# Performance work log

Measured on AMD Instinct MI355X. Metric: run time of the kernel, lower is better.

Reference implementation:

```python
import jax, jax.numpy as jnp
from jax import lax
import numpy as np

SLOPE = 0.1  # LeakyReLU negative slope used throughout DA_conv


def setup_inputs() -> dict:
    key = jax.random.key(0)
    ks = jax.random.split(key, 8)
    B, C, H, W = 16, 64, 160, 160
    Cout, red = 64, 8
    feat = jax.random.normal(ks[0], (B, C, H, W), dtype=jnp.float32)
    deg = jax.random.normal(ks[1], (B, C, 1, 1), dtype=jnp.float32)
    W1 = jax.random.normal(ks[2], (64, C), dtype=jnp.float32) * 0.05
    W2 = jax.random.normal(ks[3], (Cout * 9, 64), dtype=jnp.float32) * 0.05
    Wc = jax.random.normal(ks[4], (Cout, Cout), dtype=jnp.float32) * 0.05
    bc = jnp.zeros((Cout,), dtype=jnp.float32)
    Wd1 = jax.random.normal(ks[5], (red, C), dtype=jnp.float32) * 0.05
    Wd2 = jax.random.normal(ks[6], (Cout, red), dtype=jnp.float32) * 0.05
    return {"feat": feat, "deg": deg, "W1": W1, "W2": W2, "Wc": Wc,
            "bc": bc, "Wd1": Wd1, "Wd2": Wd2}


def reference(feat, deg, W1, W2, Wc, bc, Wd1, Wd2):
    B, C, H, W = feat.shape
    Cout = Wc.shape[0]
    KS = 3
    d = deg[:, :, 0, 0]  # [B, C]

    # --- dynamic per-sample, per-channel 3x3 kernel generation ---
    h = jax.nn.leaky_relu(d @ W1.T, SLOPE)            # [B, 64]
    k = (h @ W2.T).reshape(B * Cout, 1, KS, KS)        # [B*Cout, 1, 3, 3]

    # grouped depthwise conv: input [1, B*C, H, W], groups = B*C
    x = feat.reshape(1, B * C, H, W)
    out = lax.conv_general_dilated(
        x, k, window_strides=(1, 1), padding=[(1, 1), (1, 1)],
        dimension_numbers=("NCHW", "OIHW", "NCHW"),
        feature_group_count=B * C)
    out = jax.nn.leaky_relu(out, SLOPE).reshape(B, Cout, H, W)

    # 1x1 conv with bias (common.default_conv)
    out = jnp.einsum("oi,bihw->bohw", Wc, out) + bc[None, :, None, None]

    # --- channel attention branch (1x1 convs == matmuls on [B,C]) ---
    a = jax.nn.leaky_relu(jnp.einsum("ri,bi->br", Wd1, d), SLOPE)   # [B, red]
    att = jax.nn.sigmoid(jnp.einsum("or,br->bo", Wd2, a))           # [B, Cout]

    return out + feat * att[:, :, None, None]
```

## Files before the change

kernel.cpp:

```cpp
#include <hip/hip_runtime.h>
#include <hip/hip_bf16.h>
#include <math.h>

#define SLOPE 0.1f
#define B_ 16
#define C_ 64
#define H_ 160
#define W_ 160
#define HW_ (H_*W_)

typedef short bf16x8 __attribute__((ext_vector_type(8)));
typedef float f32x4  __attribute__((ext_vector_type(4)));
typedef unsigned int uint2v __attribute__((ext_vector_type(2)));

__device__ __forceinline__ float lrelu(float x) { return fmaxf(x, SLOPE * x); }
__device__ __forceinline__ unsigned f2bf(float x) {
  union { float f; unsigned u; } c; c.f = x;
  return (c.u + 0x7fffu + ((c.u >> 16) & 1u)) >> 16;
}
__device__ __forceinline__ float bf2f(unsigned short u) {
  union { unsigned u; float f; } c; c.u = ((unsigned)u) << 16; return c.f;
}

__device__ __forceinline__ void gl2lds16(const void* g, void* l) {
  __builtin_amdgcn_global_load_lds(
      (const __attribute__((address_space(1))) void*)g,
      (__attribute__((address_space(3))) void*)l, 16, 0, 0);
}

__global__ __launch_bounds__(64) void prep_kernel(
    const float* __restrict__ deg,
    const float* __restrict__ W1,
    const float* __restrict__ W2,
    const float* __restrict__ Wd1,
    const float* __restrict__ Wd2,
    float* __restrict__ ws) {
  const int b = blockIdx.x;
  const int j = threadIdx.x;
  __shared__ float sd[64], sh[64], sa[8];
  sd[j] = deg[b * 64 + j];
  __syncthreads();

  float acc = 0.f;
  for (int i = 0; i < 64; ++i) acc = fmaf(sd[i], W1[j * 64 + i], acc);
  sh[j] = lrelu(acc);

  if (j < 8) {
    float s = 0.f;
    for (int i = 0; i < 64; ++i) s = fmaf(sd[i], Wd1[j * 64 + i], s);
    sa[j] = lrelu(s);
  }
  __syncthreads();

  float kv[9];
#pragma unroll
  for (int t = 0; t < 9; ++t) kv[t] = 0.f;
  for (int l = 0; l < 64; ++l) {
    float hl = sh[l];
#pragma unroll
    for (int t = 0; t < 9; ++t) kv[t] = fmaf(hl, W2[(j * 9 + t) * 64 + l], kv[t]);
  }
  unsigned short* kw = (unsigned short*)(ws + 1024) + (b * 64 + j) * 16;
#pragma unroll
  for (int t = 0; t < 9; ++t) kw[t] = (unsigned short)f2bf(kv[t]);
#pragma unroll
  for (int t = 9; t < 16; ++t) kw[t] = 0;

  float s2 = 0.f;
#pragma unroll
  for (int r = 0; r < 8; ++r) s2 = fmaf(Wd2[j * 8 + r], sa[r], s2);
  ws[b * 64 + j] = 1.f / (1.f + __expf(-s2));
}

__global__ __launch_bounds__(256, 4) void main_kernel(
    const float* __restrict__ feat,
    const float* __restrict__ Wc,
    const float* __restrict__ bc,
    const float* __restrict__ ws,
    float* __restrict__ out) {
  __shared__ __align__(16) float S[2][16][240];
  __shared__ __align__(16) unsigned short Tt[2048];
  __shared__ __align__(16) unsigned short Ff[2048];
  __shared__ __align__(16) unsigned short Kl[1024];

  const int rb  = blockIdx.x;
  const int bid = (rb & 7) * 400 + (rb >> 3);
  const int b   = bid / 200;
  const int rem = bid - b * 200;
  const int ty  = rem / 10, tx = rem - ty * 10;
  const int x0 = tx * 16, y0 = ty * 8;
  const int tid = threadIdx.x;
  const int lane = tid & 63, wid = tid >> 6;

  const float* __restrict__ attp  = ws + b * 64;
  const char*  __restrict__ kb8   = (const char*)(ws + 1024) + b * 2048;
  const float* __restrict__ plane = feat + (size_t)(b * 64) * HW_;

  const int ci = tid >> 4;
  const int q  = (tid >> 2) & 3;
  const int h  = tid & 3;
  const int nl = lane & 15, kg = lane >> 4;
  const int ochunk = wid * 16;

  const int srow = lane / 6;
  const int schk = lane - srow * 6;
  const int grow = min(max(y0 + srow - 1, 0), H_ - 1);
  const int gcol = min(max(x0 - 4 + schk * 4, 0), W_ - 4);
  const float* sp0 = plane + grow * W_ + gcol;

  union AF { bf16x8 v; unsigned short u[8]; };
  AF a[4];
#pragma unroll
  for (int g = 0; g < 4; ++g) {
    const float4 w = *(const float4*)(Wc + (ochunk + nl) * 64 + g * 16 + 4 * kg);
    a[g].u[0] = (unsigned short)f2bf(w.x); a[g].u[1] = (unsigned short)f2bf(w.y);
    a[g].u[2] = (unsigned short)f2bf(w.z); a[g].u[3] = (unsigned short)f2bf(w.w);
    a[g].u[4] = 0; a[g].u[5] = 0; a[g].u[6] = 0; a[g].u[7] = 0;
  }
  AF a2;
  {
    const unsigned short ab = (unsigned short)f2bf(attp[ochunk + nl]);
#pragma unroll
    for (int j = 0; j < 4; ++j) a2.u[j] = (nl == 4 * kg + j) ? ab : (unsigned short)0;
    a2.u[4] = 0; a2.u[5] = 0; a2.u[6] = 0; a2.u[7] = 0;
  }
  const float4 bcv = *(const float4*)(bc + ochunk + 4 * kg);

  asm volatile("s_waitcnt vmcnt(0)" ::: "memory");

  if (wid == 0) {
    gl2lds16(kb8 + lane * 16, &Kl[0]);
    gl2lds16(kb8 + 1024 + lane * 16, &Kl[512]);
  }
#define STAGE(g, bf) \
  if (lane < 60) { \
    const float* s_ = sp0 + (size_t)((g) * 16 + wid * 4) * HW_; \
    gl2lds16(s_,              &S[bf][wid * 4 + 0][0]); \
    gl2lds16(s_ + 1 * HW_,    &S[bf][wid * 4 + 1][0]); \
    gl2lds16(s_ + 2 * HW_,    &S[bf][wid * 4 + 2][0]); \
    gl2lds16(s_ + 3 * HW_,    &S[bf][wid * 4 + 3][0]); \
  }
  STAGE(0, 0);

  f32x4 acc[8];
#pragma unroll
  for (int nt = 0; nt < 8; ++nt) acc[nt] = (f32x4){0.f, 0.f, 0.f, 0.f};

  const float mlz = (x0 == 0 && q == 0) ? 0.f : 1.f;
  const float mrz = (x0 == W_ - 16 && q == 3) ? 0.f : 1.f;

  const unsigned t_base = (unsigned)(uintptr_t)&Tt[0] + (unsigned)(lane * 8);
  const unsigned f_base = (unsigned)(uintptr_t)&Ff[0] + (unsigned)(lane * 8);
  union BU { bf16x8 v; uint2v qv[2]; };

#pragma unroll
  for (int g = 0; g < 4; ++g) {
    const int bf = g & 1;
    if (g < 3) { STAGE(g + 1, bf ^ 1); }
    if (g < 3) asm volatile("s_waitcnt vmcnt(4)" ::: "memory");
    else       asm volatile("s_waitcnt vmcnt(0)" ::: "memory");
    __builtin_amdgcn_s_barrier();
    __builtin_amdgcn_sched_barrier(0);

    const unsigned short* kr = &Kl[(g * 16 + ci) * 16];
    union KU { uint4 v; unsigned short u[8]; } k07;
    k07.v = *(const uint4*)kr;
    const unsigned short k8u = kr[8];
    float kk[9];
#pragma unroll
    for (int t = 0; t < 8; ++t) kk[t] = bf2f(k07.u[t]);
    kk[8] = bf2f(k8u);

    float rv[4][9];
#pragma unroll
    for (int rr = 0; rr < 4; ++rr) {
      const float* sp = &S[bf][ci][(2 * h + rr) * 24 + 4 * q];
      const f32x4 v0 = *(const f32x4*)sp;
      const f32x4 v1 = *(const f32x4*)(sp + 4);
      rv[rr][0] = v0[0]; rv[rr][1] = v0[1]; rv[rr][2] = v0[2];
      rv[rr][3] = v0[3] * mlz;
      rv[rr][4] = v1[0]; rv[rr][5] = v1[1]; rv[rr][6] = v1[2]; rv[rr][7] = v1[3];
      rv[rr][8] = sp[8] * mrz;
    }

#pragma unroll
    for (int rr = 0; rr < 2; ++rr) {
      const int srw = 2 * h + rr;
      const float mt = (srw == 0 && y0 == 0) ? 0.f : 1.f;
      const float mb = (srw == 7 && y0 == H_ - 8) ? 0.f : 1.f;
      float sv[4], fv[4];
#pragma unroll
      for (int j = 0; j < 4; ++j) {
        float ts = fmaf(rv[rr][j + 5], kk[2], fmaf(rv[rr][j + 4], kk[1], rv[rr][j + 3] * kk[0]));
        float cs = fmaf(rv[rr + 1][j + 5], kk[5], fmaf(rv[rr + 1][j + 4], kk[4], rv[rr + 1][j + 3] * kk[3]));
        float bs = fmaf(rv[rr + 2][j + 5], kk[8], fmaf(rv[rr + 2][j + 4], kk[7], rv[rr + 2][j + 3] * kk[6]));
        sv[j] = fmaf(mt, ts, fmaf(mb, bs, cs));
        fv[j] = rv[rr + 1][j + 4];
      }
      uint2v tq, fq;
      tq.x = f2bf(lrelu(sv[0])) | (f2bf(lrelu(sv[1])) << 16);
      tq.y = f2bf(lrelu(sv[2])) | (f2bf(lrelu(sv[3])) << 16);
      fq.x = f2bf(fv[0]) | (f2bf(fv[1]) << 16);
      fq.y = f2bf(fv[2]) | (f2bf(fv[3]) << 16);
      const int tidx = srw * 256 + ci * 16 + 4 * q;
      *(uint2v*)&Tt[tidx] = tq;
      *(uint2v*)&Ff[tidx] = fq;
    }

    asm volatile("s_waitcnt lgkmcnt(0)" ::: "memory");
    __builtin_amdgcn_s_barrier();
    __builtin_amdgcn_sched_barrier(0);

    uint2v tr[8];
#pragma unroll
    for (int nt = 0; nt < 8; ++nt)
      asm volatile("ds_read_b64_tr_b16 %0, %1 offset:%2"
                   : "=v"(tr[nt]) : "v"(t_base), "i"(nt * 512));
    if (wid == g) {
      uint2v fr[8];
#pragma unroll
      for (int nt = 0; nt < 8; ++nt)
        asm volatile("ds_read_b64_tr_b16 %0, %1 offset:%2"
                     : "=v"(fr[nt]) : "v"(f_base), "i"(nt * 512));
      asm volatile("s_waitcnt lgkmcnt(8)" ::: "memory");
      __builtin_amdgcn_sched_barrier(0);
#pragma unroll
      for (int nt = 0; nt < 8; ++nt) {
        BU bu; bu.qv[0] = tr[nt]; bu.qv[1] = (uint2v){0u, 0u};
        acc[nt] = __builtin_amdgcn_mfma_f32_16x16x32_bf16(a[g].v, bu.v, acc[nt], 0, 0, 0);
      }
      asm volatile("s_waitcnt lgkmcnt(0)" ::: "memory");
      __builtin_amdgcn_sched_barrier(0);
#pragma unroll
      for (int nt = 0; nt < 8; ++nt) {
        BU bu; bu.qv[0] = fr[nt]; bu.qv[1] = (uint2v){0u, 0u};
        acc[nt] = __builtin_amdgcn_mfma_f32_16x16x32_bf16(a2.v, bu.v, acc[nt], 0, 0, 0);
      }
    } else {
      asm volatile("s_waitcnt lgkmcnt(0)" ::: "memory");
      __builtin_amdgcn_sched_barrier(0);
#pragma unroll
      for (int nt = 0; nt < 8; ++nt) {
        BU bu; bu.qv[0] = tr[nt]; bu.qv[1] = (uint2v){0u, 0u};
        acc[nt] = __builtin_amdgcn_mfma_f32_16x16x32_bf16(a[g].v, bu.v, acc[nt], 0, 0, 0);
      }
    }
    __builtin_amdgcn_s_barrier();
    __builtin_amdgcn_sched_barrier(0);
  }
#undef STAGE

  const int ob = ochunk + 4 * kg;
  float* __restrict__ outb = out + (size_t)(b * 64) * HW_;
#pragma unroll
  for (int nt = 0; nt < 8; ++nt) {
    const int off = (y0 + nt) * W_ + x0 + nl;
    outb[(size_t)(ob + 0) * HW_ + off] = acc[nt][0] + bcv.x;
    outb[(size_t)(ob + 1) * HW_ + off] = acc[nt][1] + bcv.y;
    outb[(size_t)(ob + 2) * HW_ + off] = acc[nt][2] + bcv.z;
    outb[(size_t)(ob + 3) * HW_ + off] = acc[nt][3] + bcv.w;
  }
}

extern "C" void kernel_launch(void* const* d_in, const int* in_sizes, int n_in,
                              void* d_out, int out_size, void* d_ws, size_t ws_size,
                              hipStream_t stream) {
  const float* feat = (const float*)d_in[0];
  const float* deg  = (const float*)d_in[1];
  const float* W1   = (const float*)d_in[2];
  const float* W2   = (const float*)d_in[3];
  const float* Wc   = (const float*)d_in[4];
  const float* bc   = (const float*)d_in[5];
  const float* Wd1  = (const float*)d_in[6];
  const float* Wd2  = (const float*)d_in[7];
  float* out = (float*)d_out;
  float* ws  = (float*)d_ws;

  prep_kernel<<<dim3(B_), dim3(64), 0, stream>>>(deg, W1, W2, Wd1, Wd2, ws);
  main_kernel<<<dim3(3200), dim3(256), 0, stream>>>(feat, Wc, bc, ws, out);
}
```

Baseline: 74.13 us.

## Apply attention residual in fp32 epilogue and double-buffer depthwise tile to drop barrier

Drops the Ff bf16 feature tile and the extra MFMA pass with the diagonal attention matrix. The owning wave now reads residual feature values straight from the fp32 staging buffer and adds feat*att in the epilogue with an FMA, which also keeps the residual in full precision. The Tt buffer is double-buffered by stage parity so the barrier at the top of each iteration can go, and the per-sample kernel weights are repacked into a compact 12-element per-wave layout. This costs 32 extra registers for the residual and more LDS for the doubled Tt, and depends on the barrier reordering staying race-free.

```diff
diff --git a/kernel.cpp b/kernel.cpp
--- a/kernel.cpp
+++ b/kernel.cpp
@@ -60,11 +60,11 @@
 #pragma unroll
     for (int t = 0; t < 9; ++t) kv[t] = fmaf(hl, W2[(j * 9 + t) * 64 + l], kv[t]);
   }
-  unsigned short* kw = (unsigned short*)(ws + 1024) + (b * 64 + j) * 16;
+  const int slot = ((j & 15) >> 2) * 16 + (j >> 4) * 4 + (j & 3);
+  unsigned short* kw = (unsigned short*)((char*)ws + 4096) + b * 768 + slot * 12;
 #pragma unroll
   for (int t = 0; t < 9; ++t) kw[t] = (unsigned short)f2bf(kv[t]);
-#pragma unroll
-  for (int t = 9; t < 16; ++t) kw[t] = 0;
+  kw[9] = 0; kw[10] = 0; kw[11] = 0;
 
   float s2 = 0.f;
 #pragma unroll
@@ -78,10 +78,9 @@
     const float* __restrict__ bc,
     const float* __restrict__ ws,
     float* __restrict__ out) {
-  __shared__ __align__(16) float S[2][16][240];
-  __shared__ __align__(16) unsigned short Tt[2048];
-  __shared__ __align__(16) unsigned short Ff[2048];
-  __shared__ __align__(16) unsigned short Kl[1024];
+  __shared__ __align__(16) float S[2][16][244];
+  __shared__ __align__(16) unsigned short Tt[4096];
+  __shared__ __align__(16) unsigned short Kl[768];
 
   const int rb  = blockIdx.x;
   const int bid = (rb & 7) * 400 + (rb >> 3);
@@ -93,7 +92,7 @@
   const int lane = tid & 63, wid = tid >> 6;
 
   const float* __restrict__ attp  = ws + b * 64;
-  const char*  __restrict__ kb8   = (const char*)(ws + 1024) + b * 2048;
+  const char*  __restrict__ kb8   = (const char*)ws + 4096 + b * 1536;
   const float* __restrict__ plane = feat + (size_t)(b * 64) * HW_;
 
   const int ci = tid >> 4;
@@ -112,69 +111,70 @@
   AF a[4];
 #pragma unroll
   for (int g = 0; g < 4; ++g) {
-    const float4 w = *(const float4*)(Wc + (ochunk + nl) * 64 + g * 16 + 4 * kg);
-    a[g].u[0] = (unsigned short)f2bf(w.x); a[g].u[1] = (unsigned short)f2bf(w.y);
-    a[g].u[2] = (unsigned short)f2bf(w.z); a[g].u[3] = (unsigned short)f2bf(w.w);
+    const f32x4 w = *(const f32x4*)(Wc + (ochunk + nl) * 64 + g * 16 + 4 * kg);
+    a[g].u[0] = (unsigned short)f2bf(w[0]); a[g].u[1] = (unsigned short)f2bf(w[1]);
+    a[g].u[2] = (unsigned short)f2bf(w[2]); a[g].u[3] = (unsigned short)f2bf(w[3]);
     a[g].u[4] = 0; a[g].u[5] = 0; a[g].u[6] = 0; a[g].u[7] = 0;
   }
-  AF a2;
-  {
-    const unsigned short ab = (unsigned short)f2bf(attp[ochunk + nl]);
-#pragma unroll
-    for (int j = 0; j < 4; ++j) a2.u[j] = (nl == 4 * kg + j) ? ab : (unsigned short)0;
-    a2.u[4] = 0; a2.u[5] = 0; a2.u[6] = 0; a2.u[7] = 0;
-  }
-  const float4 bcv = *(const float4*)(bc + ochunk + 4 * kg);
-
+  const f32x4 bcv = *(const f32x4*)(bc + ochunk + 4 * kg);
+  const f32x4 atv = *(const f32x4*)(attp + ochunk + 4 * kg);
+  asm volatile("" :: "v"(a[0].v), "v"(a[1].v), "v"(a[2].v), "v"(a[3].v),
+                     "v"(bcv), "v"(atv));
   asm volatile("s_waitcnt vmcnt(0)" ::: "memory");
 
-  if (wid == 0) {
-    gl2lds16(kb8 + lane * 16, &Kl[0]);
-    gl2lds16(kb8 + 1024 + lane * 16, &Kl[512]);
-  }
-#define STAGE(g, bf) \
+  if (lane < 24) gl2lds16(kb8 + wid * 384 + lane * 16, &Kl[wid * 192]);
+#define STAGE(g_, bf_) \
   if (lane < 60) { \
-    const float* s_ = sp0 + (size_t)((g) * 16 + wid * 4) * HW_; \
-    gl2lds16(s_,              &S[bf][wid * 4 + 0][0]); \
-    gl2lds16(s_ + 1 * HW_,    &S[bf][wid * 4 + 1][0]); \
-    gl2lds16(s_ + 2 * HW_,    &S[bf][wid * 4 + 2][0]); \
-    gl2lds16(s_ + 3 * HW_,    &S[bf][wid * 4 + 3][0]); \
+    const float* s_ = sp0 + (size_t)((g_) * 16 + wid * 4) * HW_; \
+    gl2lds16(s_,            &S[bf_][wid * 4 + 0][0]); \
+    gl2lds16(s_ + HW_,      &S[bf_][wid * 4 + 1][0]); \
+    gl2lds16(s_ + 2 * HW_,  &S[bf_][wid * 4 + 2][0]); \
+    gl2lds16(s_ + 3 * HW_,  &S[bf_][wid * 4 + 3][0]); \
   }
   STAGE(0, 0);
 
   f32x4 acc[8];
 #pragma unroll
   for (int nt = 0; nt < 8; ++nt) acc[nt] = (f32x4){0.f, 0.f, 0.f, 0.f};
+  float resid[8][4];
+#pragma unroll
+  for (int nt = 0; nt < 8; ++nt)
+#pragma unroll
+    for (int j = 0; j < 4; ++j) resid[nt][j] = 0.f;
 
   const float mlz = (x0 == 0 && q == 0) ? 0.f : 1.f;
   const float mrz = (x0 == W_ - 16 && q == 3) ? 0.f : 1.f;
 
-  const unsigned t_base = (unsigned)(uintptr_t)&Tt[0] + (unsigned)(lane * 8);
-  const unsigned f_base = (unsigned)(uintptr_t)&Ff[0] + (unsigned)(lane * 8);
+  const unsigned t_lds0 = (unsigned)(uintptr_t)&Tt[0] + (unsigned)(lane * 8);
+  const unsigned t_lds1 = t_lds0 + 4096u;
   union BU { bf16x8 v; uint2v qv[2]; };
 
 #pragma unroll
   for (int g = 0; g < 4; ++g) {
-    const int bf = g & 1;
-    if (g < 3) { STAGE(g + 1, bf ^ 1); }
-    if (g < 3) asm volatile("s_waitcnt vmcnt(4)" ::: "memory");
-    else       asm volatile("s_waitcnt vmcnt(0)" ::: "memory");
-    __builtin_amdgcn_s_barrier();
-    __builtin_amdgcn_sched_barrier(0);
-
-    const unsigned short* kr = &Kl[(g * 16 + ci) * 16];
-    union KU { uint4 v; unsigned short u[8]; } k07;
-    k07.v = *(const uint4*)kr;
+    const int sb = g & 1;
+    if (g < 3) {
+      STAGE(g + 1, (g + 1) & 1);
+      asm volatile("s_waitcnt vmcnt(4)" ::: "memory");
+    } else {
+      asm volatile("s_waitcnt vmcnt(0)" ::: "memory");
+    }
+    __builtin_amdgcn_sched_barrier(0);
+
+    const unsigned short* kr = &Kl[wid * 192 + g * 48 + (lane >> 4) * 12];
+    union KU { uint2v v; unsigned short u[4]; };
+    KU kA, kB;
+    kA.v = *(const uint2v*)(kr);
+    kB.v = *(const uint2v*)(kr + 4);
     const unsigned short k8u = kr[8];
     float kk[9];
 #pragma unroll
-    for (int t = 0; t < 8; ++t) kk[t] = bf2f(k07.u[t]);
+    for (int t = 0; t < 4; ++t) { kk[t] = bf2f(kA.u[t]); kk[4 + t] = bf2f(kB.u[t]); }
     kk[8] = bf2f(k8u);
 
     float rv[4][9];
 #pragma unroll
     for (int rr = 0; rr < 4; ++rr) {
-      const float* sp = &S[bf][ci][(2 * h + rr) * 24 + 4 * q];
+      const float* sp = &S[sb][ci][(2 * h + rr) * 24 + 4 * q];
       const f32x4 v0 = *(const f32x4*)sp;
       const f32x4 v1 = *(const f32x4*)(sp + 4);
       rv[rr][0] = v0[0]; rv[rr][1] = v0[1]; rv[rr][2] = v0[2];
@@ -188,26 +188,22 @@
       const int srw = 2 * h + rr;
       const float mt = (srw == 0 && y0 == 0) ? 0.f : 1.f;
       const float mb = (srw == 7 && y0 == H_ - 8) ? 0.f : 1.f;
-      float sv[4], fv[4];
+      float sv[4];
 #pragma unroll
       for (int j = 0; j < 4; ++j) {
         float ts = fmaf(rv[rr][j + 5], kk[2], fmaf(rv[rr][j + 4], kk[1], rv[rr][j + 3] * kk[0]));
         float cs = fmaf(rv[rr + 1][j + 5], kk[5], fmaf(rv[rr + 1][j + 4], kk[4], rv[rr + 1][j + 3] * kk[3]));
         float bs = fmaf(rv[rr + 2][j + 5], kk[8], fmaf(rv[rr + 2][j + 4], kk[7], rv[rr + 2][j + 3] * kk[6]));
         sv[j] = fmaf(mt, ts, fmaf(mb, bs, cs));
-        fv[j] = rv[rr + 1][j + 4];
       }
-      uint2v tq, fq;
+      uint2v tq;
       tq.x = f2bf(lrelu(sv[0])) | (f2bf(lrelu(sv[1])) << 16);
       tq.y = f2bf(lrelu(sv[2])) | (f2bf(lrelu(sv[3])) << 16);
-      fq.x = f2bf(fv[0]) | (f2bf(fv[1]) << 16);
-      fq.y = f2bf(fv[2]) | (f2bf(fv[3]) << 16);
-      const int tidx = srw * 256 + ci * 16 + 4 * q;
-      *(uint2v*)&Tt[tidx] = tq;
-      *(uint2v*)&Ff[tidx] = fq;
+      *(uint2v*)&Tt[sb * 2048 + srw * 256 + ci * 16 + 4 * q] = tq;
     }
 
     asm volatile("s_waitcnt lgkmcnt(0)" ::: "memory");
+    __builtin_amdgcn_sched_barrier(0);
     __builtin_amdgcn_s_barrier();
     __builtin_amdgcn_sched_barrier(0);
 
@@ -215,38 +211,28 @@
 #pragma unroll
     for (int nt = 0; nt < 8; ++nt)
       asm volatile("ds_read_b64_tr_b16 %0, %1 offset:%2"
-                   : "=v"(tr[nt]) : "v"(t_base), "i"(nt * 512));
+                   : "=v"(tr[nt]) : "v"(sb ? t_lds1 : t_lds0), "i"(nt * 512));
+
     if (wid == g) {
-      uint2v fr[8];
+      volatile const float* Sv = &S[sb][0][0];
 #pragma unroll
       for (int nt = 0; nt < 8; ++nt)
-        asm volatile("ds_read_b64_tr_b16 %0, %1 offset:%2"
-                     : "=v"(fr[nt]) : "v"(f_base), "i"(nt * 512));
-      asm volatile("s_waitcnt lgkmcnt(8)" ::: "memory");
-      __builtin_amdgcn_sched_barrier(0);
-#pragma unroll
-      for (int nt = 0; nt < 8; ++nt) {
-        BU bu; bu.qv[0] = tr[nt]; bu.qv[1] = (uint2v){0u, 0u};
-        acc[nt] = __builtin_amdgcn_mfma_f32_16x16x32_bf16(a[g].v, bu.v, acc[nt], 0, 0, 0);
-      }
+#pragma unroll
+        for (int j = 0; j < 4; ++j)
+          resid[nt][j] = Sv[(4 * kg + j) * 244 + (nt + 1) * 24 + 4 + nl];
       asm volatile("s_waitcnt lgkmcnt(0)" ::: "memory");
-      __builtin_amdgcn_sched_barrier(0);
-#pragma unroll
-      for (int nt = 0; nt < 8; ++nt) {
-        BU bu; bu.qv[0] = fr[nt]; bu.qv[1] = (uint2v){0u, 0u};
-        acc[nt] = __builtin_amdgcn_mfma_f32_16x16x32_bf16(a2.v, bu.v, acc[nt], 0, 0, 0);
-      }
-    } else {
-      asm volatile("s_waitcnt lgkmcnt(0)" ::: "memory");
-      __builtin_amdgcn_sched_barrier(0);
-#pragma unroll
-      for (int nt = 0; nt < 8; ++nt) {
-        BU bu; bu.qv[0] = tr[nt]; bu.qv[1] = (uint2v){0u, 0u};
-        acc[nt] = __builtin_amdgcn_mfma_f32_16x16x32_bf16(a[g].v, bu.v, acc[nt], 0, 0, 0);
-      }
-    }
+    }
+    __builtin_amdgcn_sched_barrier(0);
     __builtin_amdgcn_s_barrier();
     __builtin_amdgcn_sched_barrier(0);
+    asm volatile("s_waitcnt lgkmcnt(0)" ::: "memory");
+    __builtin_amdgcn_sched_barrier(0);
+
+#pragma unroll
+    for (int nt = 0; nt < 8; ++nt) {
+      BU bu; bu.qv[0] = tr[nt]; bu.qv[1] = (uint2v){0u, 0u};
+      acc[nt] = __builtin_amdgcn_mfma_f32_16x16x32_bf16(a[g].v, bu.v, acc[nt], 0, 0, 0);
+    }
   }
 #undef STAGE
 
@@ -255,10 +241,10 @@
 #pragma unroll
   for (int nt = 0; nt < 8; ++nt) {
     const int off = (y0 + nt) * W_ + x0 + nl;
-    outb[(size_t)(ob + 0) * HW_ + off] = acc[nt][0] + bcv.x;
-    outb[(size_t)(ob + 1) * HW_ + off] = acc[nt][1] + bcv.y;
-    outb[(size_t)(ob + 2) * HW_ + off] = acc[nt][2] + bcv.z;
-    outb[(size_t)(ob + 3) * HW_ + off] = acc[nt][3] + bcv.w;
+    outb[(size_t)(ob + 0) * HW_ + off] = fmaf(resid[nt][0], atv[0], acc[nt][0] + bcv[0]);
+    outb[(size_t)(ob + 1) * HW_ + off] = fmaf(resid[nt][1], atv[1], acc[nt][1] + bcv[1]);
+    outb[(size_t)(ob + 2) * HW_ + off] = fmaf(resid[nt][2], atv[2], acc[nt][2] + bcv[2]);
+    outb[(size_t)(ob + 3) * HW_ + off] = fmaf(resid[nt][3], atv[3], acc[nt][3] + bcv[3]);
   }
 }
 
```

Result: slower. 116.0 us (+56.5%).
